# Performance work log

Measured on AMD Instinct MI355X. Metric: run time of the kernel, lower is better.

Reference implementation:

```python
import jax, jax.numpy as jnp
import numpy as np

# SE(3)-equivariant CNN (e3nn/se3cnn-style). The steerable-kernel basis (Clebsch-
# Gordan angular solutions x radial profiles) is a FIXED, non-learned tensor; its
# generating code was not provided, so we use a deterministic random stand-in
# basis of the same shape/contraction structure: kernel = einsum(weights, basis).

K = 7          # conv kernel size
STRIDE = 2
PAD = 3
EPS = 1e-5
BLOCKS = [
    dict(so=8,  vo=4, si=1,  vi=0),
    dict(so=8,  vo=4, si=8,  vi=4),
    dict(so=16, vo=4, si=8,  vi=4),
    dict(so=64, vo=0, si=16, vi=4),
]

def rs_in(b):
    r = [(b['si'], 1)]
    if b['vi'] > 0:
        r += [(b['vi'], 3), (b['vi'], 9)]   # scalars, vectors, 3x3 tensors
    return r

def rs_out(b):
    r = [(b['so'], 1)]
    if b['vo'] > 0:
        r += [(b['vo'], 3)]
    return r

def n_basis(do, di):
    return 3 * min(do, di)   # 3 radial profiles x angular paths (stand-in count)

def _make_bases():
    bases = {}
    for bi, b in enumerate(BLOCKS):
        for oi, (_, do) in enumerate(rs_out(b)):
            for ii, (_, di) in enumerate(rs_in(b)):
                nb = n_basis(do, di)
                rng = np.random.RandomState(1000 * bi + 10 * oi + ii)
                arr = rng.randn(nb, do, di, K, K, K).astype(np.float32)
                bases[(bi, oi, ii)] = jnp.asarray(arr / np.sqrt(nb * di * K ** 3))
    return bases

BASES = _make_bases()

def assemble_kernel(bi, ws):
    b = BLOCKS[bi]
    rows, k = [], 0
    for oi, (mo, do) in enumerate(rs_out(b)):
        cols = []
        for ii, (mi, di) in enumerate(rs_in(b)):
            basis = BASES[(bi, oi, ii)]  # [nb, do, di, K, K, K]
            blk = jnp.einsum('oin,nabxyz->oaibxyz', ws[k], basis)
            cols.append(blk.reshape(mo * do, mi * di, K, K, K))
            k += 1
        rows.append(jnp.concatenate(cols, axis=1))
    return jnp.concatenate(rows, axis=0)  # [C_out, C_in, K, K, K]

def block_forward(bi, x, ws, g_s, g_v, bias):
    b = BLOCKS[bi]
    si, vi, so, vo = b['si'], b['vi'], b['so'], b['vo']
    if vi > 0:  # TensorProduct: outer product of each vector field with itself
        B, _, D, H, W = x.shape
        v = x[:, si:si + 3 * vi].reshape(B, vi, 3, D, H, W)
        t = jnp.einsum('bvixyz,bvjxyz->bvijxyz', v, v).reshape(B, vi * 9, D, H, W)
        x = jnp.concatenate([x, t], axis=1)
    kern = assemble_kernel(bi, ws)
    y = jax.lax.conv_general_dilated(x, kern, (STRIDE,) * 3, [(PAD, PAD)] * 3,
                                     dimension_numbers=('NCDHW', 'OIDHW', 'NCDHW'))
    # SE3BatchNorm (training stats) + BiasRelu (relu on scalars only)
    s = y[:, :so]
    m = s.mean(axis=(0, 2, 3, 4), keepdims=True)
    var = ((s - m) ** 2).mean(axis=(0, 2, 3, 4), keepdims=True)
    s = (s - m) / jnp.sqrt(var + EPS) * g_s[None, :, None, None, None]
    s = jax.nn.relu(s + bias[None, :, None, None, None])
    if vo > 0:
        B2, _, D2, H2, W2 = y.shape
        v = y[:, so:].reshape(B2, vo, 3, D2, H2, W2)
        n2 = (v ** 2).sum(axis=2).mean(axis=(0, 2, 3, 4))  # [vo] mean field norm^2
        v = v / jnp.sqrt(n2 + EPS)[None, :, None, None, None, None]
        v = v * g_v[None, :, None, None, None, None]
        return jnp.concatenate([s, v.reshape(B2, vo * 3, D2, H2, W2)], axis=1)
    return s

def _forward(x, w0_0, w0_1, w1_0, w1_1, w1_2, w1_3, w1_4, w1_5,
             w2_0, w2_1, w2_2, w2_3, w2_4, w2_5, w3_0, w3_1, w3_2,
             g0_s, g0_v, g1_s, g1_v, g2_s, g2_v, g3_s,
             bias0, bias1, bias2, bias3, bn_g, bn_b, lin_w, lin_b):
    ws = [[w0_0, w0_1], [w1_0, w1_1, w1_2, w1_3, w1_4, w1_5],
          [w2_0, w2_1, w2_2, w2_3, w2_4, w2_5], [w3_0, w3_1, w3_2]]
    g_s = [g0_s, g1_s, g2_s, g3_s]
    g_v = [g0_v, g1_v, g2_v, None]
    bias = [bias0, bias1, bias2, bias3]
    # bn_in: BatchNorm3d(1, affine=False), training stats
    m = x.mean(axis=(0, 2, 3, 4), keepdims=True)
    v = ((x - m) ** 2).mean(axis=(0, 2, 3, 4), keepdims=True)
    x = (x - m) / jnp.sqrt(v + EPS)
    for bi in range(4):
        x = block_forward(bi, x, ws[bi], g_s[bi], g_v[bi], bias[bi])
    x = x.mean(axis=(2, 3, 4))  # global spatial mean -> [B, 64]
    mu = x.mean(axis=0, keepdims=True)
    var = ((x - mu) ** 2).mean(axis=0, keepdims=True)
    x = (x - mu) / jnp.sqrt(var + EPS) * bn_g + bn_b
    return x @ lin_w + lin_b

def setup_inputs():
    key = jax.random.key(0)
    ki = [0]
    def nk():
        ki[0] += 1
        return jax.random.fold_in(key, ki[0])
    inp = {'x': jax.random.normal(nk(), (16, 1, 64, 64, 64), dtype=jnp.float32)}
    for bi, b in enumerate(BLOCKS):
        j = 0
        for (mo, do) in rs_out(b):
            for (mi, di) in rs_in(b):
                nb = n_basis(do, di)
                inp[f'w{bi}_{j}'] = 0.2 * jax.random.normal(nk(), (mo, mi, nb), dtype=jnp.float32)
                j += 1
        inp[f'g{bi}_s'] = jnp.ones((b['so'],), jnp.float32)
        if b['vo'] > 0:
            inp[f'g{bi}_v'] = jnp.ones((b['vo'],), jnp.float32)
        inp[f'bias{bi}'] = jnp.zeros((b['so'],), jnp.float32)
    inp['bn_g'] = jnp.ones((64,), jnp.float32)
    inp['bn_b'] = jnp.zeros((64,), jnp.float32)
    inp['lin_w'] = 0.1 * jax.random.normal(nk(), (64, 10), dtype=jnp.float32)
    inp['lin_b'] = jnp.zeros((10,), jnp.float32)
    return inp

def reference(x, w0_0, w0_1, w1_0, w1_1, w1_2, w1_3, w1_4, w1_5,
              w2_0, w2_1, w2_2, w2_3, w2_4, w2_5, w3_0, w3_1, w3_2,
              g0_s, g0_v, g1_s, g1_v, g2_s, g2_v, g3_s,
              bias0, bias1, bias2, bias3, bn_g, bn_b, lin_w, lin_b):
    return _forward(x, w0_0, w0_1, w1_0, w1_1, w1_2, w1_3, w1_4, w1_5,
                    w2_0, w2_1, w2_2, w2_3, w2_4, w2_5, w3_0, w3_1, w3_2,
                    g0_s, g0_v, g1_s, g1_v, g2_s, g2_v, g3_s,
                    bias0, bias1, bias2, bias3, bn_g, bn_b, lin_w, lin_b)
```

## Files before the change

### kernel.cpp

```cpp
#include <hip/hip_runtime.h>
#include <cmath>

constexpr long XN_OFF   = 0;
constexpr long Y0_OFF   = 4194304;
constexpr long Y1_OFF   = 14680064;
constexpr long Y2_OFF   = 15990784;
constexpr long Y3_OFF   = 16220160;
constexpr long K0_OFF   = 16285696;
constexpr long K1_OFF   = 16293536;
constexpr long K2_OFF   = 16732576;
constexpr long K3_OFF   = 17347232;
constexpr long BAS_OFF  = 18952864;
constexpr long SCR_OFF  = 19225552;
constexpr long PARTD_OFF = 20182872;
constexpr long SSD_OFF   = 20191064;
constexpr long ISTD_OFF  = 20191320;
constexpr long POOLD_OFF = 20191324;
constexpr long CNT_OFF   = 20193372;
constexpr long GBASE_OFF = 20193644;

constexpr int PGRP = 4096;
constexpr int MAXG = 16;

struct GenDesc {
  double sdiv[17];
  int seed[17], n[17], scr_off[17], L[17], basis_off[17];
};
struct AsmDesc {
  const float* w[17];
  int cum[18];
  int basis_off[17], row_off[17], col_off[17];
  int dd[17], di[17], mi[17], nb[17], citot[17];
  long koff[17];
};

__global__ __launch_bounds__(256)
void mt_fill_kernel(unsigned int* __restrict__ scratch, GenDesc d) {
  __shared__ unsigned int mt[624];
  const int bb = blockIdx.x;
  const int tid = threadIdx.x;
  if (tid == 0) {
    unsigned int s = (unsigned int)d.seed[bb];
    for (int pos = 0; pos < 624; pos++) {
      mt[pos] = s;
      s = 1812433253u * (s ^ (s >> 30)) + (unsigned)pos + 1u;
    }
  }
  __syncthreads();
  unsigned int* out = scratch + d.scr_off[bb];
  const int L = d.L[bb];
  const int ntw = (L + 623) / 624;
  for (int t = 0; t < ntw; t++) {
    unsigned int v1 = 0, v2 = 0;
    if (tid < 227) { v1 = mt[tid]; v2 = mt[tid + 1]; }
    __syncthreads();
    if (tid < 227) {
      unsigned int y = (v1 & 0x80000000u) | (v2 & 0x7fffffffu);
      mt[tid] = mt[tid + 397] ^ (y >> 1) ^ ((y & 1u) ? 0x9908b0dfu : 0u);
    }
    __syncthreads();
    if (tid < 227) { v1 = mt[227 + tid]; v2 = mt[228 + tid]; }
    __syncthreads();
    if (tid < 227) {
      unsigned int y = (v1 & 0x80000000u) | (v2 & 0x7fffffffu);
      mt[227 + tid] = mt[tid] ^ (y >> 1) ^ ((y & 1u) ? 0x9908b0dfu : 0u);
    }
    __syncthreads();
    if (tid < 170) {
      int i = 454 + tid;
      v1 = mt[i]; v2 = (i < 623) ? mt[i + 1] : mt[0];
    }
    __syncthreads();
    if (tid < 170) {
      int i = 454 + tid;
      unsigned int y = (v1 & 0x80000000u) | (v2 & 0x7fffffffu);
      mt[i] = mt[i - 227] ^ (y >> 1) ^ ((y & 1u) ? 0x9908b0dfu : 0u);
    }
    __syncthreads();
    const int base = t * 624;
    for (int j = tid; j < 624; j += 256) {
      if (base + j < L) {
        unsigned int y = mt[j];
        y ^= y >> 11;
        y ^= (y << 7) & 0x9d2c5680u;
        y ^= (y << 15) & 0xefc60000u;
        y ^= y >> 18;
        out[base + j] = y;
      }
    }
    __syncthreads();
  }
}

__device__ inline bool polar_accept(const unsigned int* src, int p,
                                    double& x1, double& x2, double& r2) {
  unsigned int w0 = src[4 * p], w1 = src[4 * p + 1], w2 = src[4 * p + 2], w3 = src[4 * p + 3];
  double u1 = ((double)(w0 >> 5) * 67108864.0 + (double)(w1 >> 6)) * (1.0 / 9007199254740992.0);
  double u2 = ((double)(w2 >> 5) * 67108864.0 + (double)(w3 >> 6)) * (1.0 / 9007199254740992.0);
  x1 = 2.0 * u1 - 1.0; x2 = 2.0 * u2 - 1.0;
  r2 = x1 * x1 + x2 * x2;
  return (r2 < 1.0) && (r2 != 0.0);
}

__global__ __launch_bounds__(256)
void polar_count_kernel(const unsigned int* __restrict__ scratch, int* __restrict__ counts,
                        GenDesc d) {
  const int bb = blockIdx.y, grp = blockIdx.x, tid = threadIdx.x;
  const unsigned int* src = scratch + d.scr_off[bb];
  const int P = d.L[bb] >> 2;
  const int p0 = grp * PGRP;
  int cnt = 0;
  if (p0 < P) {
    const int p1 = min(p0 + PGRP, P);
    for (int p = p0 + tid; p < p1; p += 256) {
      double x1, x2, r2;
      if (polar_accept(src, p, x1, x2, r2)) cnt++;
    }
  }
  #pragma unroll
  for (int o = 32; o > 0; o >>= 1) cnt += __shfl_down(cnt, o);
  __shared__ int ws4[4];
  if ((tid & 63) == 0) ws4[tid >> 6] = cnt;
  __syncthreads();
  if (tid == 0) counts[bb * MAXG + grp] = ws4[0] + ws4[1] + ws4[2] + ws4[3];
}

__global__ void polar_scan_kernel(const int* __restrict__ counts, int* __restrict__ gbase) {
  int bb = threadIdx.x;
  if (bb < 17) {
    int acc = 0;
    for (int g = 0; g < MAXG; g++) {
      gbase[bb * MAXG + g] = acc;
      acc += counts[bb * MAXG + g];
    }
  }
}

__global__ __launch_bounds__(256)
void polar_write_kernel(const unsigned int* __restrict__ scratch, const int* __restrict__ gbase,
                        float* __restrict__ bases, GenDesc d) {
  const int bb = blockIdx.y, grp = blockIdx.x;
  const int tid = threadIdx.x;
  const int lane = tid & 63, wid = tid >> 6;
  const unsigned int* src = scratch + d.scr_off[bb];
  float* out = bases + d.basis_off[bb];
  const int n = d.n[bb];
  const int need = (n + 1) >> 1;
  const int P = d.L[bb] >> 2;
  const int p0 = grp * PGRP;
  if (p0 >= P) return;
  int base = gbase[bb * MAXG + grp];
  if (base >= need) return;
  const double sdiv = d.sdiv[bb];
  const int p1 = min(p0 + PGRP, P);
  __shared__ int lds_tot[4];
  for (int ch = p0; ch < p1 && base < need; ch += 256) {
    const int p = ch + tid;
    bool accept = false;
    double x1 = 0.0, x2 = 0.0, r2 = 0.0;
    if (p < p1) accept = polar_accept(src, p, x1, x2, r2);
    unsigned long long mask = __ballot(accept ? 1 : 0);
    int prefix = __popcll(mask & ((1ull << lane) - 1ull));
    int tot = __popcll(mask);
    if (lane == 0) lds_tot[wid] = tot;
    __syncthreads();
    int waveoff = 0;
    #pragma unroll
    for (int w = 0; w < 4; w++) waveoff += (w < wid) ? lds_tot[w] : 0;
    int tot_all = lds_tot[0] + lds_tot[1] + lds_tot[2] + lds_tot[3];
    if (accept) {
      int k = base + waveoff + prefix;
      double f = sqrt(-2.0 * log(r2) / r2);
      int i0 = 2 * k, i1 = 2 * k + 1;
      if (i0 < n) { float g = (float)(f * x2); out[i0] = (float)((double)g / sdiv); }
      if (i1 < n) { float g = (float)(f * x1); out[i1] = (float)((double)g / sdiv); }
    }
    base += tot_all;
    __syncthreads();
  }
}

__global__ void assemble_kernel(const float* __restrict__ bases, float* __restrict__ ws, AsmDesc d) {
  int g = blockIdx.x * 256 + threadIdx.x;
  if (g >= d.cum[17]) return;
  int k = 0;
  while (g >= d.cum[k + 1]) k++;
  int l = g - d.cum[k];
  const int dd = d.dd[k], di = d.di[k], mi = d.mi[k], nb = d.nb[k];
  const int cols = mi * di;
  int tap = l % 343; int rc = l / 343;
  int c = rc % cols; int r = rc / cols;
  int o = r / dd, a = r - o * dd;
  int i = c / di, b2 = c - i * di;
  const float* wp = d.w[k];
  const float* bp = bases + d.basis_off[k] + ((a * di + b2) * 343 + tap);
  const int wbase = (o * mi + i) * nb;
  const int bstride = dd * di * 343;
  double s = 0.0;
  for (int nn = 0; nn < nb; nn++) s += (double)wp[wbase + nn] * (double)bp[(long)nn * bstride];
  int R = d.row_off[k] + r, C = d.col_off[k] + c;
  int t49 = tap / 7, kx = tap - t49 * 7;
  ws[d.koff[k] + ((long)(R * d.citot[k] + C) * 49 + t49) * 8 + kx] = (float)s;
}

template<int CI_TOT, int CO, int ISP, int OSP, int TDX, int TDY, int TDZ,
         int S, int CI_PER, bool ATOMIC, int SI, int CDIR>
__global__ __launch_bounds__(TDX*TDY*TDZ)
void conv3d_kernel(const float* __restrict__ src, const float* __restrict__ kern,
                   float* __restrict__ out) {
  constexpr int NT = TDX * TDY * TDZ;
  constexpr int TILE_X = TDX * S;
  constexpr int IN_X = 2 * TILE_X + 5, IN_Y = 2 * TDY + 5, IN_Z = 2 * TDZ + 5;
  constexpr int IN_XP = IN_X + 1;
  constexpr int IN_TOT = IN_X * IN_Y * IN_Z;
  constexpr int NTX = OSP / TILE_X, NTY = OSP / TDY;
  __shared__ float lds_in[IN_Z * IN_Y * IN_XP + 1];
  const int tid = threadIdx.x;
  const int tx = tid % TDX, ty = (tid / TDX) % TDY, tz = tid / (TDX * TDY);
  const int bx = blockIdx.x;
  const int tXi = bx % NTX, tYi = (bx / NTX) % NTY, tZi = bx / (NTX * NTY);
  const int b = blockIdx.y;
  const int ci0 = blockIdx.z * CI_PER;
  const int gx0 = 2 * (tXi * TILE_X) - 3, gy0 = 2 * (tYi * TDY) - 3, gz0 = 2 * (tZi * TDZ) - 3;

  float acc[S][CO];
  #pragma unroll
  for (int u = 0; u < S; u++)
    #pragma unroll
    for (int c = 0; c < CO; c++) acc[u][c] = 0.f;

  for (int cc = 0; cc < CI_PER; cc++) {
    const int ci = ci0 + cc;
    for (int l = tid; l < IN_TOT; l += NT) {
      int dx = l % IN_X; int t2 = l / IN_X; int dy = t2 % IN_Y; int dz = t2 / IN_Y;
      int gx = gx0 + dx, gy = gy0 + dy, gz = gz0 + dz;
      float v = 0.f;
      if ((unsigned)gx < (unsigned)ISP && (unsigned)gy < (unsigned)ISP &&
          (unsigned)gz < (unsigned)ISP) {
        long spi = ((long)gz * ISP + gy) * ISP + gx;
        if (ci < CDIR) {
          v = src[(long)(b * CDIR + ci) * ISP * ISP * ISP + spi];
        } else {
          int r = ci - CDIR; int vv = r / 9; int ij = r - vv * 9;
          int i2 = ij / 3, j2 = ij - i2 * 3;
          float va = src[(long)(b * CDIR + SI + 3 * vv + i2) * ISP * ISP * ISP + spi];
          float vb = src[(long)(b * CDIR + SI + 3 * vv + j2) * ISP * ISP * ISP + spi];
          v = va * vb;
        }
      }
      int r = dz * IN_Y + dy;
      lds_in[r * IN_XP + dx + ((r >> 1) & 1)] = v;
    }
    __syncthreads();
    float part[S][CO];
    #pragma unroll
    for (int u = 0; u < S; u++)
      #pragma unroll
      for (int c2 = 0; c2 < CO; c2++) part[u][c2] = 0.f;
    for (int kz = 0; kz < 7; kz++) {
      for (int ky = 0; ky < 7; ky++) {
        const int r = (2 * tz + kz) * IN_Y + (2 * ty + ky);
        const int rowbase = r * IN_XP + ((r >> 1) & 1) + 2 * S * tx;
        float strip[2 * S + 5];
        #pragma unroll
        for (int j = 0; j < 2 * S + 5; j++) strip[j] = lds_in[rowbase + j];
        const long wrow0 = (long)ci * 392 + (kz * 7 + ky) * 8;
        #pragma unroll
        for (int c2 = 0; c2 < CO; c2++) {
          const float* __restrict__ wrow = kern + wrow0 + (long)c2 * CI_TOT * 392;
          const float4 wa = *(const float4*)(wrow);
          const float4 wb = *(const float4*)(wrow + 4);
          const float wk[7] = {wa.x, wa.y, wa.z, wa.w, wb.x, wb.y, wb.z};
          #pragma unroll
          for (int kx = 0; kx < 7; kx++) {
            #pragma unroll
            for (int u = 0; u < S; u++)
              part[u][c2] += strip[2 * u + kx] * wk[kx];
          }
        }
      }
    }
    #pragma unroll
    for (int u = 0; u < S; u++)
      #pragma unroll
      for (int c2 = 0; c2 < CO; c2++) acc[u][c2] += part[u][c2];
    __syncthreads();
  }
  const int ozg = tZi * TDZ + tz, oyg = tYi * TDY + ty;
  #pragma unroll
  for (int u = 0; u < S; u++) {
    const int oxg = tXi * TILE_X + tx * S + u;
    #pragma unroll
    for (int co = 0; co < CO; co++) {
      long idx = (((long)(b * CO + co) * OSP + ozg) * OSP + oyg) * OSP + oxg;
      if (ATOMIC) atomicAdd(&out[idx], acc[u][co]);
      else out[idx] = acc[u][co];
    }
  }
}

__global__ __launch_bounds__(256)
void conv_b3_kernel(const float* __restrict__ src, const float* __restrict__ k3,
                    float* __restrict__ out) {
  constexpr int CLS = 580;
  __shared__ float lds_in[16 * CLS];
  const int tid = threadIdx.x;
  const int s = tid & 63, w = tid >> 6;
  const int ox = s & 3, oy = (s >> 2) & 3, oz = s >> 4;
  const int b = blockIdx.y;
  const int cogrp = blockIdx.x >> 2, cch = blockIdx.x & 3;
  const int co0 = cogrp * 16 + w * 4;
  for (int l = tid; l < 16 * 512; l += 256) {
    int cl = l >> 9, sp = l & 511;
    int ci = cch * 16 + cl;
    float v;
    if (ci < 28) v = src[(long)(b * 28 + ci) * 512 + sp];
    else {
      int r = ci - 28; int vv = r / 9; int ij = r - vv * 9;
      int i2 = ij / 3, j2 = ij - i2 * 3;
      v = src[(long)(b * 28 + 16 + 3 * vv + i2) * 512 + sp] *
          src[(long)(b * 28 + 16 + 3 * vv + j2) * 512 + sp];
    }
    int r = sp >> 3;
    lds_in[cl * CLS + r * 9 + (sp & 7) + ((r >> 1) & 1)] = v;
  }
  __syncthreads();
  float acc[4] = {0.f, 0.f, 0.f, 0.f};
  for (int cl = 0; cl < 16; cl++) {
    const int ci = cch * 16 + cl;
    float part[4] = {0.f, 0.f, 0.f, 0.f};
    for (int kz = 0; kz < 7; kz++) {
      const int iz = 2 * oz + kz - 3;
      const bool vz = (unsigned)iz < 8u;
      for (int ky = 0; ky < 7; ky++) {
        const int iy = 2 * oy + ky - 3;
        const bool vyz = vz && ((unsigned)iy < 8u);
        const int r = iz * 8 + iy;
        const int rowbase = cl * CLS + r * 9 + ((r >> 1) & 1);
        float strip[7];
        #pragma unroll
        for (int kx = 0; kx < 7; kx++) {
          const int ix = 2 * ox + kx - 3;
          strip[kx] = (vyz && (unsigned)ix < 8u) ? lds_in[rowbase + ix] : 0.f;
        }
        #pragma unroll
        for (int j = 0; j < 4; j++) {
          const float* __restrict__ wr =
              k3 + ((long)((co0 + j) * 64 + ci) * 49 + (kz * 7 + ky)) * 8;
          const float4 wa = *(const float4*)(wr);
          const float4 wb = *(const float4*)(wr + 4);
          const float wk[7] = {wa.x, wa.y, wa.z, wa.w, wb.x, wb.y, wb.z};
          #pragma unroll
          for (int kx = 0; kx < 7; kx++) part[j] += strip[kx] * wk[kx];
        }
      }
    }
    #pragma unroll
    for (int j = 0; j < 4; j++) acc[j] += part[j];
  }
  #pragma unroll
  for (int j = 0; j < 4; j++)
    atomicAdd(&out[(long)(b * 64 + co0 + j) * 64 + s], acc[j]);
}

__device__ inline void block_reduce2d(double& s, double& q) {
  #pragma unroll
  for (int o = 32; o > 0; o >>= 1) { s += __shfl_down(s, o); q += __shfl_down(q, o); }
  __shared__ double ls[8];
  const int lane = threadIdx.x & 63, wid = threadIdx.x >> 6;
  if (lane == 0) { ls[wid * 2] = s; ls[wid * 2 + 1] = q; }
  __syncthreads();
  if (threadIdx.x == 0) {
    for (int w = 1; w < 4; w++) { s += ls[w * 2]; q += ls[w * 2 + 1]; }
  }
}

__global__ __launch_bounds__(256)
void in_part_kernel(const float* __restrict__ x, double* __restrict__ part) {
  double s = 0.0, q = 0.0;
  const long base = (long)blockIdx.x * 4096;
  for (int i = threadIdx.x; i < 4096; i += 256) {
    double v = (double)x[base + i]; s += v; q += v * v;
  }
  block_reduce2d(s, q);
  if (threadIdx.x == 0) { part[blockIdx.x * 2] = s; part[blockIdx.x * 2 + 1] = q; }
}

__global__ __launch_bounds__(256)
void in_final_kernel(const double* __restrict__ part, double* __restrict__ st) {
  double s = 0.0, q = 0.0;
  for (int i = threadIdx.x; i < 1024; i += 256) { s += part[i * 2]; q += part[i * 2 + 1]; }
  block_reduce2d(s, q);
  if (threadIdx.x == 0) {
    const double invN = 1.0 / 4194304.0;
    double m = s * invN;
    double var = q * invN - m * m;
    st[0] = m; st[1] = 1.0 / sqrt(var + 1e-5);
  }
}

__global__ void in_apply_kernel(const float* __restrict__ x, const double* __restrict__ st,
                                float* __restrict__ xn) {
  long i = (long)blockIdx.x * 256 + threadIdx.x;
  if (i < 4194304) xn[i] = (float)(((double)x[i] - st[0]) * st[1]);
}

__global__ __launch_bounds__(256)
void stats_partial_kernel(const float* __restrict__ y, double* __restrict__ part,
                          int C, int SP, int P) {
  const int c = blockIdx.x / P, p = blockIdx.x % P;
  const int chunk = SP / P;
  double s = 0.0, q = 0.0;
  for (int b = 0; b < 16; b++) {
    const float* base = y + (long)(b * C + c) * SP + (long)p * chunk;
    for (int i = threadIdx.x; i < chunk; i += 256) {
      double v = (double)base[i]; s += v; q += v * v;
    }
  }
  block_reduce2d(s, q);
  if (threadIdx.x == 0) { part[blockIdx.x * 2] = s; part[blockIdx.x * 2 + 1] = q; }
}

__global__ __launch_bounds__(256)
void stats_final_kernel(const double* __restrict__ part, double* __restrict__ ss,
                        const float* __restrict__ g_s, const float* __restrict__ g_v,
                        const float* __restrict__ bias, int C, int P, int so, double invcount) {
  __shared__ double lsq[64];
  const int c = threadIdx.x;
  double s = 0.0, q = 0.0;
  if (c < C) {
    for (int p = 0; p < P; p++) { s += part[(c * P + p) * 2]; q += part[(c * P + p) * 2 + 1]; }
    lsq[c] = q;
  }
  __syncthreads();
  if (c < C) {
    if (c < so) {
      double m = s * invcount;
      double var = q * invcount - m * m;
      double rstd = 1.0 / sqrt(var + 1e-5);
      double sc = (double)g_s[c] * rstd;
      ss[c * 2] = sc; ss[c * 2 + 1] = (double)bias[c] - m * sc;
    } else {
      int v = (c - so) / 3;
      double n2 = (lsq[so + 3 * v] + lsq[so + 3 * v + 1] + lsq[so + 3 * v + 2]) * invcount;
      ss[c * 2] = (double)g_v[v] / sqrt(n2 + 1e-5);
      ss[c * 2 + 1] = 0.0;
    }
  }
}

__global__ void apply_kernel(float* __restrict__ y, const double* __restrict__ ss,
                             int C, int SP, int so, long total) {
  long idx = (long)blockIdx.x * 256 + threadIdx.x;
  if (idx >= total) return;
  int c = (int)((idx / SP) % C);
  double v = (double)y[idx] * ss[c * 2] + ss[c * 2 + 1];
  if (c < so) v = fmax(v, 0.0);
  y[idx] = (float)v;
}

__global__ void pool_kernel(const float* __restrict__ y3, double* __restrict__ pooled) {
  int t = blockIdx.x * 256 + threadIdx.x;
  if (t < 1024) {
    double s = 0.0;
    for (int i = 0; i < 64; i++) s += (double)y3[(long)t * 64 + i];
    pooled[t] = s * (1.0 / 64.0);
  }
}

__global__ __launch_bounds__(256)
void head_kernel(const double* __restrict__ pooled, const float* __restrict__ bn_g,
                 const float* __restrict__ bn_b, const float* __restrict__ lin_w,
                 const float* __restrict__ lin_b, float* __restrict__ out) {
  __shared__ double p[1024];
  for (int i = threadIdx.x; i < 1024; i += 256) p[i] = pooled[i];
  __syncthreads();
  if (threadIdx.x < 64) {
    int c = threadIdx.x;
    double s = 0.0, q = 0.0;
    for (int b = 0; b < 16; b++) { double v = p[b * 64 + c]; s += v; q += v * v; }
    double m = s * (1.0 / 16.0);
    double var = q * (1.0 / 16.0) - m * m;
    double rstd = 1.0 / sqrt(var + 1e-5);
    for (int b = 0; b < 16; b++)
      p[b * 64 + c] = (p[b * 64 + c] - m) * rstd * (double)bn_g[c] + (double)bn_b[c];
  }
  __syncthreads();
  if (threadIdx.x < 160) {
    int b = threadIdx.x / 10, j = threadIdx.x - b * 10;
    double s = (double)lin_b[j];
    for (int c = 0; c < 64; c++) s += p[b * 64 + c] * (double)lin_w[c * 10 + j];
    out[b * 10 + j] = (float)s;
  }
}

extern "C" void kernel_launch(void* const* d_in, const int* in_sizes, int n_in,
                              void* d_out, int out_size, void* d_ws, size_t ws_size,
                              hipStream_t stream) {
  (void)in_sizes; (void)n_in; (void)out_size; (void)ws_size;
  float* W = (float*)d_ws;
  double* PARTD = (double*)(W + PARTD_OFF);
  double* SSD   = (double*)(W + SSD_OFF);
  double* ISTD  = (double*)(W + ISTD_OFF);
  double* POOLD = (double*)(W + POOLD_OFF);
  int* CNT   = (int*)(W + CNT_OFF);
  int* GBASE = (int*)(W + GBASE_OFF);

  static const int k_bi[17]  = {0,0, 1,1,1,1,1,1, 2,2,2,2,2,2, 3,3,3};
  static const int k_oi[17]  = {0,1, 0,0,0,1,1,1, 0,0,0,1,1,1, 0,0,0};
  static const int k_ii[17]  = {0,0, 0,1,2,0,1,2, 0,1,2,0,1,2, 0,1,2};
  static const int k_do[17]  = {1,3, 1,1,1,3,3,3, 1,1,1,3,3,3, 1,1,1};
  static const int k_dI[17]  = {1,1, 1,3,9,1,3,9, 1,3,9,1,3,9, 1,3,9};
  static const int k_mo[17]  = {8,4, 8,8,8,4,4,4, 16,16,16,4,4,4, 64,64,64};
  static const int k_mi[17]  = {1,1, 8,4,4,8,4,4, 8,4,4,8,4,4, 16,4,4};
  static const int k_row[17] = {0,8, 0,0,0,8,8,8, 0,0,0,16,16,16, 0,0,0};
  static const int k_col[17] = {0,0, 0,8,20,0,8,20, 0,8,20,0,8,20, 0,16,28};
  static const int k_win[17] = {1,2, 6,7,8,9,10,11, 15,16,17,18,19,20, 24,25,26};
  static const int citot_by_bi[4] = {1, 56, 56, 64};
  static const long koff_by_bi[4] = {K0_OFF, K1_OFF, K2_OFF, K3_OFF};

  GenDesc gd;
  AsmDesc ad;
  int scr = 0, boff = 0, cum = 0;
  ad.cum[0] = 0;
  for (int k = 0; k < 17; k++) {
    int bi = k_bi[k];
    int dd = k_do[k], di = k_dI[k];
    int nb = 3 * (dd < di ? dd : di);
    int n = nb * dd * di * 343;
    gd.seed[k] = 1000 * bi + 10 * k_oi[k] + k_ii[k];
    gd.n[k] = n;
    int P = (3 * n) / 4 + 2048;
    gd.L[k] = 4 * P;
    gd.scr_off[k] = scr; scr += gd.L[k];
    gd.basis_off[k] = boff; boff += n;
    gd.sdiv[k] = sqrt((double)(nb * di * 343));
    ad.w[k] = (const float*)d_in[k_win[k]];
    ad.basis_off[k] = gd.basis_off[k];
    ad.row_off[k] = k_row[k]; ad.col_off[k] = k_col[k];
    ad.dd[k] = dd; ad.di[k] = di; ad.mi[k] = k_mi[k]; ad.nb[k] = nb;
    ad.citot[k] = citot_by_bi[bi];
    ad.koff[k] = koff_by_bi[bi];
    cum += k_mo[k] * dd * k_mi[k] * di * 343;
    ad.cum[k + 1] = cum;
  }

  const float* x     = (const float*)d_in[0];
  const float* g0_s  = (const float*)d_in[3];
  const float* g0_v  = (const float*)d_in[4];
  const float* bias0 = (const float*)d_in[5];
  const float* g1_s  = (const float*)d_in[12];
  const float* g1_v  = (const float*)d_in[13];
  const float* bias1 = (const float*)d_in[14];
  const float* g2_s  = (const float*)d_in[21];
  const float* g2_v  = (const float*)d_in[22];
  const float* bias2 = (const float*)d_in[23];
  const float* g3_s  = (const float*)d_in[27];
  const float* bias3 = (const float*)d_in[28];
  const float* bn_g  = (const float*)d_in[29];
  const float* bn_b  = (const float*)d_in[30];
  const float* lin_w = (const float*)d_in[31];
  const float* lin_b = (const float*)d_in[32];

  hipMemsetAsync(W + Y1_OFF, 0, 1310720 * 4, stream);
  hipMemsetAsync(W + Y2_OFF, 0, 229376 * 4, stream);
  hipMemsetAsync(W + Y3_OFF, 0, 65536 * 4, stream);

  mt_fill_kernel<<<17, 256, 0, stream>>>((unsigned int*)(W + SCR_OFF), gd);
  polar_count_kernel<<<dim3(MAXG, 17), 256, 0, stream>>>((const unsigned int*)(W + SCR_OFF),
                                                         CNT, gd);
  polar_scan_kernel<<<1, 32, 0, stream>>>(CNT, GBASE);
  polar_write_kernel<<<dim3(MAXG, 17), 256, 0, stream>>>((const unsigned int*)(W + SCR_OFF),
                                                         GBASE, W + BAS_OFF, gd);
  assemble_kernel<<<(cum + 255) / 256, 256, 0, stream>>>(W + BAS_OFF, W, ad);

  in_part_kernel<<<1024, 256, 0, stream>>>(x, PARTD);
  in_final_kernel<<<1, 256, 0, stream>>>(PARTD, ISTD);
  in_apply_kernel<<<16384, 256, 0, stream>>>(x, ISTD, W + XN_OFF);

  conv3d_kernel<1, 20, 64, 32, 4, 8, 8, 2, 1, false, 0, 1>
      <<<dim3(64, 16, 1), 256, 0, stream>>>(W + XN_OFF, W + K0_OFF, W + Y0_OFF);
  stats_partial_kernel<<<20 * 32, 256, 0, stream>>>(W + Y0_OFF, PARTD, 20, 32768, 32);
  stats_final_kernel<<<1, 256, 0, stream>>>(PARTD, SSD, g0_s, g0_v, bias0,
                                            20, 32, 8, 1.0 / 524288.0);
  apply_kernel<<<40960, 256, 0, stream>>>(W + Y0_OFF, SSD, 20, 32768, 8, 10485760L);

  conv3d_kernel<56, 20, 32, 16, 4, 8, 8, 2, 7, true, 8, 20>
      <<<dim3(8, 16, 8), 256, 0, stream>>>(W + Y0_OFF, W + K1_OFF, W + Y1_OFF);
  stats_partial_kernel<<<20 * 8, 256, 0, stream>>>(W + Y1_OFF, PARTD, 20, 4096, 8);
  stats_final_kernel<<<1, 256, 0, stream>>>(PARTD, SSD, g1_s, g1_v, bias1,
                                            20, 8, 8, 1.0 / 65536.0);
  apply_kernel<<<5120, 256, 0, stream>>>(W + Y1_OFF, SSD, 20, 4096, 8, 1310720L);

  conv3d_kernel<56, 28, 16, 8, 4, 8, 4, 2, 4, true, 8, 20>
      <<<dim3(2, 16, 14), 128, 0, stream>>>(W + Y1_OFF, W + K2_OFF, W + Y2_OFF);
  stats_partial_kernel<<<28 * 2, 256, 0, stream>>>(W + Y2_OFF, PARTD, 28, 512, 2);
  stats_final_kernel<<<1, 256, 0, stream>>>(PARTD, SSD, g2_s, g2_v, bias2,
                                            28, 2, 16, 1.0 / 8192.0);
  apply_kernel<<<896, 256, 0, stream>>>(W + Y2_OFF, SSD, 28, 512, 16, 229376L);

  conv_b3_kernel<<<dim3(16, 16), 256, 0, stream>>>(W + Y2_OFF, W + K3_OFF, W + Y3_OFF);
  stats_partial_kernel<<<64, 256, 0, stream>>>(W + Y3_OFF, PARTD, 64, 64, 1);
  stats_final_kernel<<<1, 256, 0, stream>>>(PARTD, SSD, g3_s, nullptr, bias3,
                                            64, 1, 64, 1.0 / 1024.0);
  apply_kernel<<<256, 256, 0, stream>>>(W + Y3_OFF, SSD, 64, 64, 64, 65536L);

  pool_kernel<<<4, 256, 0, stream>>>(W + Y3_OFF, POOLD);
  head_kernel<<<1, 256, 0, stream>>>(POOLD, bn_g, bn_b, lin_w, lin_b, (float*)d_out);
}
```

Measured before the change: 2.144 ms.

## Split conv output channels across blocks and stage input one kz slab at a time

The conv kernel now splits output channels into groups handled by separate blocks along gridDim.z, giving more blocks and fewer accumulator registers per thread. LDS staging is restructured so only the depth slab needed for the current kz tap is loaded. This shrinks shared memory and should raise occupancy, at the cost of more barriers per input channel and recomputing the tensor-product inputs once per output-channel group. Block 2's launch geometry is also retuned: no input-channel chunking and a larger depth tile.

Result: no change. 2.146 ms (+0.1%).

```diff
diff --git a/kernel.cpp b/kernel.cpp
--- a/kernel.cpp
+++ b/kernel.cpp
@@ -203,70 +203,75 @@
   ws[d.koff[k] + ((long)(R * d.citot[k] + C) * 49 + t49) * 8 + kx] = (float)s;
 }
 
-template<int CI_TOT, int CO, int ISP, int OSP, int TDX, int TDY, int TDZ,
+template<int CI_TOT, int COG, int CO_TOT, int ISP, int OSP, int TDX, int TDY, int TDZ,
          int S, int CI_PER, bool ATOMIC, int SI, int CDIR>
 __global__ __launch_bounds__(TDX*TDY*TDZ)
 void conv3d_kernel(const float* __restrict__ src, const float* __restrict__ kern,
                    float* __restrict__ out) {
   constexpr int NT = TDX * TDY * TDZ;
   constexpr int TILE_X = TDX * S;
-  constexpr int IN_X = 2 * TILE_X + 5, IN_Y = 2 * TDY + 5, IN_Z = 2 * TDZ + 5;
+  constexpr int IN_X = 2 * TILE_X + 5, IN_Y = 2 * TDY + 5;
   constexpr int IN_XP = IN_X + 1;
-  constexpr int IN_TOT = IN_X * IN_Y * IN_Z;
+  constexpr int SLAB = TDZ * IN_Y * IN_X;
   constexpr int NTX = OSP / TILE_X, NTY = OSP / TDY;
-  __shared__ float lds_in[IN_Z * IN_Y * IN_XP + 1];
+  constexpr int NCICH = CI_TOT / CI_PER;
+  __shared__ float lds_in[TDZ * IN_Y * IN_XP + 2];
   const int tid = threadIdx.x;
   const int tx = tid % TDX, ty = (tid / TDX) % TDY, tz = tid / (TDX * TDY);
   const int bx = blockIdx.x;
   const int tXi = bx % NTX, tYi = (bx / NTX) % NTY, tZi = bx / (NTX * NTY);
   const int b = blockIdx.y;
-  const int ci0 = blockIdx.z * CI_PER;
+  const int zi = blockIdx.z;
+  const int cich = zi % NCICH, cog = zi / NCICH;
+  const int ci0 = cich * CI_PER;
+  const int co0 = cog * COG;
   const int gx0 = 2 * (tXi * TILE_X) - 3, gy0 = 2 * (tYi * TDY) - 3, gz0 = 2 * (tZi * TDZ) - 3;
 
-  float acc[S][CO];
+  float acc[S][COG];
   #pragma unroll
   for (int u = 0; u < S; u++)
     #pragma unroll
-    for (int c = 0; c < CO; c++) acc[u][c] = 0.f;
+    for (int c = 0; c < COG; c++) acc[u][c] = 0.f;
 
   for (int cc = 0; cc < CI_PER; cc++) {
     const int ci = ci0 + cc;
-    for (int l = tid; l < IN_TOT; l += NT) {
-      int dx = l % IN_X; int t2 = l / IN_X; int dy = t2 % IN_Y; int dz = t2 / IN_Y;
-      int gx = gx0 + dx, gy = gy0 + dy, gz = gz0 + dz;
-      float v = 0.f;
-      if ((unsigned)gx < (unsigned)ISP && (unsigned)gy < (unsigned)ISP &&
-          (unsigned)gz < (unsigned)ISP) {
-        long spi = ((long)gz * ISP + gy) * ISP + gx;
-        if (ci < CDIR) {
-          v = src[(long)(b * CDIR + ci) * ISP * ISP * ISP + spi];
-        } else {
-          int r = ci - CDIR; int vv = r / 9; int ij = r - vv * 9;
-          int i2 = ij / 3, j2 = ij - i2 * 3;
-          float va = src[(long)(b * CDIR + SI + 3 * vv + i2) * ISP * ISP * ISP + spi];
-          float vb = src[(long)(b * CDIR + SI + 3 * vv + j2) * ISP * ISP * ISP + spi];
-          v = va * vb;
-        }
-      }
-      int r = dz * IN_Y + dy;
-      lds_in[r * IN_XP + dx + ((r >> 1) & 1)] = v;
-    }
-    __syncthreads();
-    float part[S][CO];
+    float part[S][COG];
     #pragma unroll
     for (int u = 0; u < S; u++)
       #pragma unroll
-      for (int c2 = 0; c2 < CO; c2++) part[u][c2] = 0.f;
+      for (int c2 = 0; c2 < COG; c2++) part[u][c2] = 0.f;
     for (int kz = 0; kz < 7; kz++) {
+      __syncthreads();
+      for (int l = tid; l < SLAB; l += NT) {
+        int dx = l % IN_X; int t2 = l / IN_X; int dy = t2 % IN_Y; int pz = t2 / IN_Y;
+        int gx = gx0 + dx, gy = gy0 + dy, gz = gz0 + 2 * pz + kz;
+        float v = 0.f;
+        if ((unsigned)gx < (unsigned)ISP && (unsigned)gy < (unsigned)ISP &&
+            (unsigned)gz < (unsigned)ISP) {
+          long spi = ((long)gz * ISP + gy) * ISP + gx;
+          if (ci < CDIR) {
+            v = src[(long)(b * CDIR + ci) * ISP * ISP * ISP + spi];
+          } else {
+            int r = ci - CDIR; int vv = r / 9; int ij = r - vv * 9;
+            int i2 = ij / 3, j2 = ij - i2 * 3;
+            float va = src[(long)(b * CDIR + SI + 3 * vv + i2) * ISP * ISP * ISP + spi];
+            float vb = src[(long)(b * CDIR + SI + 3 * vv + j2) * ISP * ISP * ISP + spi];
+            v = va * vb;
+          }
+        }
+        int r = pz * IN_Y + dy;
+        lds_in[r * IN_XP + dx + ((r >> 1) & 1)] = v;
+      }
+      __syncthreads();
       for (int ky = 0; ky < 7; ky++) {
-        const int r = (2 * tz + kz) * IN_Y + (2 * ty + ky);
+        const int r = tz * IN_Y + 2 * ty + ky;
         const int rowbase = r * IN_XP + ((r >> 1) & 1) + 2 * S * tx;
         float strip[2 * S + 5];
         #pragma unroll
         for (int j = 0; j < 2 * S + 5; j++) strip[j] = lds_in[rowbase + j];
-        const long wrow0 = (long)ci * 392 + (kz * 7 + ky) * 8;
+        const long wrow0 = ((long)co0 * CI_TOT + ci) * 392 + (kz * 7 + ky) * 8;
         #pragma unroll
-        for (int c2 = 0; c2 < CO; c2++) {
+        for (int c2 = 0; c2 < COG; c2++) {
           const float* __restrict__ wrow = kern + wrow0 + (long)c2 * CI_TOT * 392;
           const float4 wa = *(const float4*)(wrow);
           const float4 wb = *(const float4*)(wrow + 4);
@@ -283,18 +288,17 @@
     #pragma unroll
     for (int u = 0; u < S; u++)
       #pragma unroll
-      for (int c2 = 0; c2 < CO; c2++) acc[u][c2] += part[u][c2];
-    __syncthreads();
+      for (int c2 = 0; c2 < COG; c2++) acc[u][c2] += part[u][c2];
   }
   const int ozg = tZi * TDZ + tz, oyg = tYi * TDY + ty;
   #pragma unroll
   for (int u = 0; u < S; u++) {
     const int oxg = tXi * TILE_X + tx * S + u;
     #pragma unroll
-    for (int co = 0; co < CO; co++) {
-      long idx = (((long)(b * CO + co) * OSP + ozg) * OSP + oyg) * OSP + oxg;
-      if (ATOMIC) atomicAdd(&out[idx], acc[u][co]);
-      else out[idx] = acc[u][co];
+    for (int c2 = 0; c2 < COG; c2++) {
+      long idx = (((long)(b * CO_TOT + co0 + c2) * OSP + ozg) * OSP + oyg) * OSP + oxg;
+      if (ATOMIC) atomicAdd(&out[idx], acc[u][c2]);
+      else out[idx] = acc[u][c2];
     }
   }
 }
@@ -578,22 +582,22 @@
   in_final_kernel<<<1, 256, 0, stream>>>(PARTD, ISTD);
   in_apply_kernel<<<16384, 256, 0, stream>>>(x, ISTD, W + XN_OFF);
 
-  conv3d_kernel<1, 20, 64, 32, 4, 8, 8, 2, 1, false, 0, 1>
-      <<<dim3(64, 16, 1), 256, 0, stream>>>(W + XN_OFF, W + K0_OFF, W + Y0_OFF);
+  conv3d_kernel<1, 10, 20, 64, 32, 4, 8, 8, 2, 1, false, 0, 1>
+      <<<dim3(64, 16, 2), 256, 0, stream>>>(W + XN_OFF, W + K0_OFF, W + Y0_OFF);
   stats_partial_kernel<<<20 * 32, 256, 0, stream>>>(W + Y0_OFF, PARTD, 20, 32768, 32);
   stats_final_kernel<<<1, 256, 0, stream>>>(PARTD, SSD, g0_s, g0_v, bias0,
                                             20, 32, 8, 1.0 / 524288.0);
   apply_kernel<<<40960, 256, 0, stream>>>(W + Y0_OFF, SSD, 20, 32768, 8, 10485760L);
 
-  conv3d_kernel<56, 20, 32, 16, 4, 8, 8, 2, 7, true, 8, 20>
-      <<<dim3(8, 16, 8), 256, 0, stream>>>(W + Y0_OFF, W + K1_OFF, W + Y1_OFF);
+  conv3d_kernel<56, 10, 20, 32, 16, 4, 8, 8, 2, 7, true, 8, 20>
+      <<<dim3(8, 16, 16), 256, 0, stream>>>(W + Y0_OFF, W + K1_OFF, W + Y1_OFF);
   stats_partial_kernel<<<20 * 8, 256, 0, stream>>>(W + Y1_OFF, PARTD, 20, 4096, 8);
   stats_final_kernel<<<1, 256, 0, stream>>>(PARTD, SSD, g1_s, g1_v, bias1,
                                             20, 8, 8, 1.0 / 65536.0);
   apply_kernel<<<5120, 256, 0, stream>>>(W + Y1_OFF, SSD, 20, 4096, 8, 1310720L);
 
-  conv3d_kernel<56, 28, 16, 8, 4, 8, 4, 2, 4, true, 8, 20>
-      <<<dim3(2, 16, 14), 128, 0, stream>>>(W + Y1_OFF, W + K2_OFF, W + Y2_OFF);
+  conv3d_kernel<56, 14, 28, 16, 8, 4, 8, 8, 2, 1, true, 8, 20>
+      <<<dim3(1, 16, 112), 256, 0, stream>>>(W + Y1_OFF, W + K2_OFF, W + Y2_OFF);
   stats_partial_kernel<<<28 * 2, 256, 0, stream>>>(W + Y2_OFF, PARTD, 28, 512, 2);
   stats_final_kernel<<<1, 256, 0, stream>>>(PARTD, SSD, g2_s, g2_v, bias2,
                                             28, 2, 16, 1.0 / 8192.0);
```
